# Performance work log

Hardware: AMD Instinct MI355X
Metric: run time of the kernel (lower is better)

## Reference

```python
import jax, jax.numpy as jnp
import numpy as np
from jax import lax

MODEL_DIM = 256
CTX_LEN = 48
CHUNK = 16
NUM_LAYERS = 4
NHEAD = 8
FF_DIM = 1024
EPS = 1e-5


def setup_inputs() -> dict:
    key = jax.random.key(0)
    ks = jax.random.split(key, 16)
    B, C, T = 16, MODEL_DIM, 1024
    s = 0.02
    inp = {
        "x": jax.random.normal(ks[0], (B, C, T), dtype=jnp.float32),
        "embedding": jax.random.normal(ks[1], (B, 2, C, 32), dtype=jnp.float32),
        "ctx_buf": jnp.zeros((B, NUM_LAYERS, CTX_LEN, C), dtype=jnp.float32),
        # per-layer stacked transformer-decoder-layer params
        "Wqkv": jax.random.normal(ks[2], (NUM_LAYERS, 3 * C, C), dtype=jnp.float32) * s,
        "bqkv": jnp.zeros((NUM_LAYERS, 3 * C), dtype=jnp.float32),
        "Wo": jax.random.normal(ks[3], (NUM_LAYERS, C, C), dtype=jnp.float32) * s,
        "bo": jnp.zeros((NUM_LAYERS, C), dtype=jnp.float32),
        "W1": jax.random.normal(ks[4], (NUM_LAYERS, FF_DIM, C), dtype=jnp.float32) * s,
        "b1": jnp.zeros((NUM_LAYERS, FF_DIM), dtype=jnp.float32),
        "W2": jax.random.normal(ks[5], (NUM_LAYERS, C, FF_DIM), dtype=jnp.float32) * s,
        "b2": jnp.zeros((NUM_LAYERS, C), dtype=jnp.float32),
        "ln1_g": jnp.ones((NUM_LAYERS, C), dtype=jnp.float32),
        "ln1_b": jnp.zeros((NUM_LAYERS, C), dtype=jnp.float32),
        "ln3_g": jnp.ones((NUM_LAYERS, C), dtype=jnp.float32),
        "ln3_b": jnp.zeros((NUM_LAYERS, C), dtype=jnp.float32),
    }
    return inp


def _layernorm(x, g, b):
    mu = jnp.mean(x, axis=-1, keepdims=True)
    var = jnp.mean(jnp.square(x - mu), axis=-1, keepdims=True)
    return (x - mu) * lax.rsqrt(var + EPS) * g + b


def _mha(q_in, kv_in, Wqkv, bqkv, Wo, bo):
    # q_in: [N, Lq, C], kv_in: [N, Lk, C]; torch nn.MultiheadAttention math (eval mode)
    C = q_in.shape[-1]
    dh = C // NHEAD
    Wq, Wk, Wv = jnp.split(Wqkv, 3, axis=0)
    bq, bk, bv = jnp.split(bqkv, 3)
    q = q_in @ Wq.T + bq
    k = kv_in @ Wk.T + bk
    v = kv_in @ Wv.T + bv
    N, Lq, _ = q.shape
    Lk = k.shape[1]
    q = q.reshape(N, Lq, NHEAD, dh)
    k = k.reshape(N, Lk, NHEAD, dh)
    v = v.reshape(N, Lk, NHEAD, dh)
    scores = jnp.einsum("nqhd,nkhd->nhqk", q, k) / jnp.sqrt(jnp.asarray(dh, q.dtype))
    attn = jax.nn.softmax(scores, axis=-1)
    out = jnp.einsum("nhqk,nkhd->nqhd", attn, v).reshape(N, Lq, C)
    return out @ Wo.T + bo


def _decoder_layer(tgt, Wqkv, bqkv, Wo, bo, W1, b1, W2, b2, ln1_g, ln1_b, ln3_g, ln3_b):
    # tgt: [N, ctx+chunk, C]; query = last `chunk` tokens; dropout=identity (eval)
    q = tgt[:, -CHUNK:, :]
    x1 = _layernorm(q + _mha(q, tgt, Wqkv, bqkv, Wo, bo), ln1_g, ln1_b)
    ff = jax.nn.relu(x1 @ W1.T + b1) @ W2.T + b2
    return _layernorm(x1 + ff, ln3_g, ln3_b)


def reference(x, embedding, ctx_buf, Wqkv, bqkv, Wo, bo, W1, b1, W2, b2,
              ln1_g, ln1_b, ln3_g, ln3_b):
    B, C, T = x.shape  # T multiple of CHUNK -> mod_pad is a no-op
    # ---- conv conditioning: per-(batch,channel) causal depthwise filter ----
    Le = embedding.shape[-1]
    filt = jnp.mean(embedding, axis=1).reshape(B * C, 1, Le)  # [B*C, 1, Le]
    inp = x.reshape(1, B * C, T)
    out = lax.conv_general_dilated(
        inp, filt, window_strides=(1,), padding=[(Le - 1, 0)],
        feature_group_count=B * C, dimension_numbers=("NCH", "OIH", "NCH"))
    output = out.reshape(B, C, T).transpose(0, 2, 1)  # [B, T, C]

    # ---- causal sliding-window decoder layers ----
    nwin = T // CHUNK
    W = CTX_LEN + CHUNK
    idx = jnp.arange(nwin)[:, None] * CHUNK + jnp.arange(W)[None, :]  # [nwin, W]
    for i in range(NUM_LAYERS):
        tgt_full = jnp.concatenate([ctx_buf[:, i], output], axis=1)  # [B, ctx+T, C]
        ctx_buf = ctx_buf.at[:, i].set(tgt_full[:, -CTX_LEN:])
        win = tgt_full[:, idx].reshape(B * nwin, W, C)  # unfold -> [B*nwin, W, C]
        chunks = _decoder_layer(win, Wqkv[i], bqkv[i], Wo[i], bo[i], W1[i], b1[i],
                                W2[i], b2[i], ln1_g[i], ln1_b[i], ln3_g[i], ln3_b[i])
        output = chunks.reshape(B, T, C)
    return output.transpose(0, 2, 1), ctx_buf
```

## Files before the change

### kernel.cpp

```cpp
#include <hip/hip_runtime.h>
#include <math.h>

#define BQ      16
#define CDIM    256
#define TLEN    1024
#define CTXL    48
#define CHUNKL  16
#define NLAYER  4
#define NHEADS  8
#define DHEAD   32
#define FFDIM   1024
#define NWIN    64
#define EXTL    1072
#define QKV_N   768

typedef __attribute__((ext_vector_type(4))) float floatx4;
typedef __attribute__((ext_vector_type(8))) __bf16 bf16x8;

__device__ __forceinline__ unsigned short f2bf(float f) {
    unsigned int u = __float_as_uint(f);
    u += 0x7fff + ((u >> 16) & 1);
    return (unsigned short)(u >> 16);
}
__device__ __forceinline__ float bf2f(unsigned short h) {
    return __uint_as_float(((unsigned int)h) << 16);
}

__global__ void f2b_multi_kernel(const float* __restrict__ p0,
                                 const float* __restrict__ p1,
                                 const float* __restrict__ p2,
                                 const float* __restrict__ p3,
                                 const float* __restrict__ p4,
                                 unsigned short* __restrict__ q0,
                                 unsigned short* __restrict__ q1,
                                 unsigned short* __restrict__ q2,
                                 unsigned short* __restrict__ q3,
                                 unsigned short* __restrict__ q4) {
    const int sizes[5] = {786432, 262144, 1048576, 1048576, 786432};
    const float* ins[5] = {p0, p1, p2, p3, p4};
    unsigned short* outs[5] = {q0, q1, q2, q3, q4};
    int seg = blockIdx.y;
    int i = (blockIdx.x * 256 + threadIdx.x) * 4;
    if (i < sizes[seg]) {
        float4 v = *(const float4*)(ins[seg] + i);
        ushort4 o;
        o.x = f2bf(v.x); o.y = f2bf(v.y); o.z = f2bf(v.z); o.w = f2bf(v.w);
        *(ushort4*)(outs[seg] + i) = o;
    }
}

__global__ void conv_kernel(const float* __restrict__ x,
                            const float* __restrict__ emb,
                            float* __restrict__ tmp) {
    int bc = blockIdx.x;
    int b = bc >> 8, c = bc & 255;
    __shared__ float xs[31 + TLEN];
    __shared__ float f[32];
    int t = threadIdx.x;
    if (t < 31) xs[t] = 0.f;
    const float* xrow = x + (size_t)bc * TLEN;
    for (int s = t; s < TLEN; s += 256) xs[31 + s] = xrow[s];
    if (t < 32) {
        const float* e0 = emb + (((size_t)b * 2 + 0) * CDIM + c) * 32;
        const float* e1 = emb + (((size_t)b * 2 + 1) * CDIM + c) * 32;
        f[t] = 0.5f * (e0[t] + e1[t]);
    }
    __syncthreads();
    float* orow = tmp + (size_t)bc * TLEN;
    for (int s = t; s < TLEN; s += 256) {
        float acc = 0.f;
#pragma unroll
        for (int l = 0; l < 32; ++l) acc += f[l] * xs[s + l];
        orow[s] = acc;
    }
}

__global__ void transpose_f2b_kernel(const float* __restrict__ in,
                                     unsigned short* __restrict__ out,
                                     float* __restrict__ ctxo,
                                     int R, int S) {
    __shared__ float tile[32][33];
    int b = blockIdx.z;
    int s0 = blockIdx.x * 32, r0 = blockIdx.y * 32;
    const float* inb = in + (size_t)b * R * S;
    unsigned short* outb = out + (size_t)b * R * S;
    int tx = threadIdx.x, ty = threadIdx.y;
    for (int i = ty; i < 32; i += 8)
        tile[i][tx] = inb[(size_t)(r0 + i) * S + s0 + tx];
    __syncthreads();
    for (int i = ty; i < 32; i += 8) {
        float v = tile[tx][i];
        int t = s0 + i, c = r0 + tx;
        outb[(size_t)t * R + c] = f2bf(v);
        if (t >= TLEN - CTXL)
            ctxo[(((size_t)b * NLAYER + 0) * CTXL + (t - (TLEN - CTXL)))
                 * CDIM + c] = v;
    }
}

__global__ void transpose_b2f_kernel(const unsigned short* __restrict__ in,
                                     float* __restrict__ out,
                                     int R, int S) {
    __shared__ float tile[32][33];
    int b = blockIdx.z;
    int s0 = blockIdx.x * 32, r0 = blockIdx.y * 32;
    const unsigned short* inb = in + (size_t)b * R * S;
    float* outb = out + (size_t)b * R * S;
    int tx = threadIdx.x, ty = threadIdx.y;
    for (int i = ty; i < 32; i += 8)
        tile[i][tx] = bf2f(inb[(size_t)(r0 + i) * S + s0 + tx]);
    __syncthreads();
    for (int i = ty; i < 32; i += 8)
        outb[(size_t)(s0 + i) * R + r0 + tx] = tile[tx][i];
}

template<int BM, int BN, int WM, int WN>
__global__ __launch_bounds__(256) void gemm_bf16_kernel(
    const unsigned short* __restrict__ A,
    const unsigned short* __restrict__ ctxb,
    int mode, int layer,
    const unsigned short* __restrict__ W,
    const float* __restrict__ bias,
    unsigned short* __restrict__ outb,
    int M, int N, int K, int relu) {
    constexpr int IA = BM / 32;
    constexpr int IB = BN / 32;
    constexpr int MT = WM / 16;
    constexpr int NTT = WN / 16;
    constexpr int NWX = BN / WN;
    __shared__ __align__(16) char smem[(BM + BN) * 128];
    char* smemA = smem;
    char* smemB = smem + BM * 128;
    int tid = threadIdx.x;
    int lane = tid & 63;
    int wid = tid >> 6;
    int ln = lane & 15, kq = lane >> 4;
    int wm = (wid / NWX) * WM, wn = (wid % NWX) * WN;
    int m0 = blockIdx.y * BM, n0 = blockIdx.x * BN;

    const unsigned short* arow[IA];
    int akc[IA];
    const unsigned short* brow[IB];
    int bkc[IB];
#pragma unroll
    for (int is = 0; is < IA; ++is) {
        int q = tid + is * 256;
        int m = q >> 3;
        akc[is] = ((q & 7) ^ (m & 7)) * 8;
        int mg = m0 + m;
        if (mode == 0) {
            arow[is] = A + (size_t)mg * K;
        } else {
            int b = mg / EXTL;
            int e = mg - b * EXTL;
            arow[is] = (e < CTXL)
                ? ctxb + (((size_t)b * NLAYER + layer) * CTXL + e) * CDIM
                : A + ((size_t)b * TLEN + (e - CTXL)) * CDIM;
        }
    }
#pragma unroll
    for (int is = 0; is < IB; ++is) {
        int q = tid + is * 256;
        int m = q >> 3;
        bkc[is] = ((q & 7) ^ (m & 7)) * 8;
        brow[is] = W + (size_t)(n0 + m) * K;
    }

    floatx4 acc[MT][NTT];
#pragma unroll
    for (int i = 0; i < MT; ++i)
#pragma unroll
        for (int j = 0; j < NTT; ++j) acc[i][j] = (floatx4){0.f, 0.f, 0.f, 0.f};

    for (int kt = 0; kt < K; kt += 64) {
#pragma unroll
        for (int is = 0; is < IA; ++is) {
            int off = (is * 256 + tid) * 16;
            __builtin_amdgcn_global_load_lds(
                (const __attribute__((address_space(1))) unsigned int*)
                    (const void*)(arow[is] + kt + akc[is]),
                (__attribute__((address_space(3))) unsigned int*)
                    (void*)(smemA + off), 16, 0, 0);
        }
#pragma unroll
        for (int is = 0; is < IB; ++is) {
            int off = (is * 256 + tid) * 16;
            __builtin_amdgcn_global_load_lds(
                (const __attribute__((address_space(1))) unsigned int*)
                    (const void*)(brow[is] + kt + bkc[is]),
                (__attribute__((address_space(3))) unsigned int*)
                    (void*)(smemB + off), 16, 0, 0);
        }
        __syncthreads();
#pragma unroll
        for (int s = 0; s < 2; ++s) {
            bf16x8 af[MT], bfv[NTT];
            int kc = s * 4 + kq;
#pragma unroll
            for (int i = 0; i < MT; ++i) {
                int ml = wm + 16 * i + ln;
                af[i] = *(const bf16x8*)(smemA + (ml * 8 + (kc ^ (ml & 7))) * 16);
            }
#pragma unroll
            for (int j = 0; j < NTT; ++j) {
                int nl = wn + 16 * j + ln;
                bfv[j] = *(const bf16x8*)(smemB + (nl * 8 + (kc ^ (nl & 7))) * 16);
            }
#pragma unroll
            for (int i = 0; i < MT; ++i)
#pragma unroll
                for (int j = 0; j < NTT; ++j)
                    acc[i][j] = __builtin_amdgcn_mfma_f32_16x16x32_bf16(
                        af[i], bfv[j], acc[i][j], 0, 0, 0);
        }
        __syncthreads();
    }

#pragma unroll
    for (int i = 0; i < MT; ++i) {
#pragma unroll
        for (int r = 0; r < 4; ++r) {
            int m = m0 + wm + 16 * i + kq * 4 + r;
#pragma unroll
            for (int j = 0; j < NTT; ++j) {
                int n = n0 + wn + 16 * j + ln;
                float v = acc[i][j][r] + bias[n];
                if (relu) v = fmaxf(v, 0.f);
                outb[(size_t)m * N + n] = f2bf(v);
            }
        }
    }
}

__global__ __launch_bounds__(256) void gemm_ln_kernel(
    const unsigned short* __restrict__ A,
    const unsigned short* __restrict__ W,
    const float* __restrict__ bias,
    const unsigned short* __restrict__ resid,
    const float* __restrict__ g,
    const float* __restrict__ beta,
    unsigned short* __restrict__ outb,
    float* __restrict__ ctxo, int clayer,
    int M, int K) {
    __shared__ __align__(16) unsigned short smA[32 * 64];
    __shared__ __align__(16) unsigned short smB[256 * 64];
    __shared__ float rsum[32][4];
    __shared__ float rsqs[32][4];
    int tid = threadIdx.x;
    int lane = tid & 63;
    int wid = tid >> 6;
    int ln = lane & 15, quad = lane >> 4;
    int wn = wid * 64;
    int m0 = blockIdx.x * 32;

    const unsigned short* arow =
        A + (size_t)(m0 + (tid >> 3)) * K + ((tid & 7) ^ ((tid >> 3) & 7)) * 8;
    const unsigned short* brow[8];
#pragma unroll
    for (int is = 0; is < 8; ++is) {
        int q = tid + is * 256;
        int mm = q >> 3;
        brow[is] = W + (size_t)mm * K + ((q & 7) ^ (mm & 7)) * 8;
    }

    floatx4 acc[2][4];
#pragma unroll
    for (int i = 0; i < 2; ++i)
#pragma unroll
        for (int j = 0; j < 4; ++j) acc[i][j] = (floatx4){0.f, 0.f, 0.f, 0.f};

    for (int kt = 0; kt < K; kt += 64) {
        __builtin_amdgcn_global_load_lds(
            (const __attribute__((address_space(1))) unsigned int*)
                (const void*)(arow + kt),
            (__attribute__((address_space(3))) unsigned int*)
                (void*)((char*)smA + tid * 16), 16, 0, 0);
#pragma unroll
        for (int is = 0; is < 8; ++is) {
            __builtin_amdgcn_global_load_lds(
                (const __attribute__((address_space(1))) unsigned int*)
                    (const void*)(brow[is] + kt),
                (__attribute__((address_space(3))) unsigned int*)
                    (void*)((char*)smB + (is * 256 + tid) * 16), 16, 0, 0);
        }
        __syncthreads();
#pragma unroll
        for (int s = 0; s < 2; ++s) {
            int kc = s * 4 + quad;
            bf16x8 af[2], bfv[4];
#pragma unroll
            for (int i = 0; i < 2; ++i) {
                int ml = 16 * i + ln;
                af[i] = *(const bf16x8*)(smA + (ml * 8 + (kc ^ (ml & 7))) * 8);
            }
#pragma unroll
            for (int j = 0; j < 4; ++j) {
                int nl = wn + 16 * j + ln;
                bfv[j] = *(const bf16x8*)(smB + (nl * 8 + (kc ^ (nl & 7))) * 8);
            }
#pragma unroll
            for (int i = 0; i < 2; ++i)
#pragma unroll
                for (int j = 0; j < 4; ++j)
                    acc[i][j] = __builtin_amdgcn_mfma_f32_16x16x32_bf16(
                        af[i], bfv[j], acc[i][j], 0, 0, 0);
        }
        __syncthreads();
    }

#pragma unroll
    for (int i = 0; i < 2; ++i)
#pragma unroll
        for (int r = 0; r < 4; ++r) {
            int m = m0 + 16 * i + quad * 4 + r;
#pragma unroll
            for (int j = 0; j < 4; ++j) {
                int n = wn + 16 * j + ln;
                acc[i][j][r] += bias[n] + bf2f(resid[(size_t)m * CDIM + n]);
            }
        }

#pragma unroll
    for (int i = 0; i < 2; ++i)
#pragma unroll
        for (int r = 0; r < 4; ++r) {
            float s1 = acc[i][0][r] + acc[i][1][r] + acc[i][2][r] + acc[i][3][r];
            float s2 = acc[i][0][r] * acc[i][0][r] + acc[i][1][r] * acc[i][1][r]
                     + acc[i][2][r] * acc[i][2][r] + acc[i][3][r] * acc[i][3][r];
#pragma unroll
            for (int off = 8; off >= 1; off >>= 1) {
                s1 += __shfl_xor(s1, off, 64);
                s2 += __shfl_xor(s2, off, 64);
            }
            if (ln == 0) {
                int row = 16 * i + quad * 4 + r;
                rsum[row][wid] = s1;
                rsqs[row][wid] = s2;
            }
        }
    __syncthreads();

#pragma unroll
    for (int i = 0; i < 2; ++i)
#pragma unroll
        for (int r = 0; r < 4; ++r) {
            int row = 16 * i + quad * 4 + r;
            float tot = rsum[row][0] + rsum[row][1] + rsum[row][2] + rsum[row][3];
            float tsq = rsqs[row][0] + rsqs[row][1] + rsqs[row][2] + rsqs[row][3];
            float mu = tot * (1.f / 256.f);
            float var = tsq * (1.f / 256.f) - mu * mu;
            float inv = rsqrtf(var + 1e-5f);
            int m = m0 + row;
            int t = m & (TLEN - 1), bb = m >> 10;
            bool wctx = (clayer >= 0) && (t >= TLEN - CTXL);
#pragma unroll
            for (int j = 0; j < 4; ++j) {
                int n = wn + 16 * j + ln;
                float y = (acc[i][j][r] - mu) * inv * g[n] + beta[n];
                outb[(size_t)m * CDIM + n] = f2bf(y);
                if (wctx)
                    ctxo[(((size_t)bb * NLAYER + clayer) * CTXL
                          + (t - (TLEN - CTXL))) * CDIM + n] = y;
            }
        }
}

__global__ __launch_bounds__(256) void attn_wo_ln_kernel(
    const unsigned short* __restrict__ QKV,
    const unsigned short* __restrict__ act,
    const unsigned short* __restrict__ Wo,
    const float* __restrict__ bo,
    const float* __restrict__ g,
    const float* __restrict__ beta,
    unsigned short* __restrict__ x1out) {
    int n = blockIdx.x, b = blockIdx.y;
    __shared__ __align__(16) unsigned short Vt[256][72];
    __shared__ __align__(16) unsigned short Pb[4][16][72];
    __shared__ __align__(16) unsigned short Ol[16][280];
    __shared__ float rsum[16][4];
    __shared__ float rsqs[16][4];
    int tid = threadIdx.x;
    int lane = tid & 63, wid = tid >> 6;
    int ln = lane & 15, quad = lane >> 4;
    int key0 = n * CHUNKL;
    const unsigned short* base = QKV + (size_t)b * EXTL * QKV_N;

    {
        int row = tid >> 2;
        int c0 = (tid & 3) * 64;
        const unsigned short* vrow =
            base + (size_t)(key0 + row) * QKV_N + 512 + c0;
#pragma unroll
        for (int s = 0; s < 8; ++s) {
            bf16x8 v = *(const bf16x8*)(vrow + 8 * s);
#pragma unroll
            for (int j = 0; j < 8; ++j)
                Vt[c0 + 8 * s + j][row] = ((const unsigned short*)&v)[j];
        }
    }
    __syncthreads();

    const float scale = 0.17677669529663687f;
#pragma unroll
    for (int hh = 0; hh < 2; ++hh) {
        int h = wid * 2 + hh;
        bf16x8 qf = *(const bf16x8*)(base
            + (size_t)(CTXL + key0 + ln) * QKV_N + h * DHEAD + quad * 8);
        floatx4 sc[4];
#pragma unroll
        for (int j = 0; j < 4; ++j) {
            bf16x8 kf = *(const bf16x8*)(base
                + (size_t)(key0 + j * 16 + ln) * QKV_N + 256
                + h * DHEAD + quad * 8);
            sc[j] = __builtin_amdgcn_mfma_f32_16x16x32_bf16(
                qf, kf, (floatx4){0.f, 0.f, 0.f, 0.f}, 0, 0, 0);
        }
        float p[4][4];
#pragma unroll
        for (int r = 0; r < 4; ++r) {
            float mx = -1e30f;
#pragma unroll
            for (int j = 0; j < 4; ++j) mx = fmaxf(mx, sc[j][r]);
            mx = fmaxf(mx, __shfl_xor(mx, 1, 64));
            mx = fmaxf(mx, __shfl_xor(mx, 2, 64));
            mx = fmaxf(mx, __shfl_xor(mx, 4, 64));
            mx = fmaxf(mx, __shfl_xor(mx, 8, 64));
            float sum = 0.f;
#pragma unroll
            for (int j = 0; j < 4; ++j) {
                float e = __expf((sc[j][r] - mx) * scale);
                p[r][j] = e;
                sum += e;
            }
            sum += __shfl_xor(sum, 1, 64);
            sum += __shfl_xor(sum, 2, 64);
            sum += __shfl_xor(sum, 4, 64);
            sum += __shfl_xor(sum, 8, 64);
            float inv = 1.f / sum;
#pragma unroll
            for (int j = 0; j < 4; ++j) p[r][j] *= inv;
        }
#pragma unroll
        for (int r = 0; r < 4; ++r)
#pragma unroll
            for (int j = 0; j < 4; ++j)
                Pb[wid][quad * 4 + r][j * 16 + ln] = f2bf(p[r][j]);
        bf16x8 pa0 = *(const bf16x8*)&Pb[wid][ln][quad * 8];
        bf16x8 pa1 = *(const bf16x8*)&Pb[wid][ln][32 + quad * 8];
#pragma unroll
        for (int jt = 0; jt < 2; ++jt) {
            bf16x8 v0 = *(const bf16x8*)&Vt[h * DHEAD + jt * 16 + ln][quad * 8];
            bf16x8 v1 = *(const bf16x8*)&Vt[h * DHEAD + jt * 16 + ln][32 + quad * 8];
            floatx4 a = __builtin_amdgcn_mfma_f32_16x16x32_bf16(
                pa0, v0, (floatx4){0.f, 0.f, 0.f, 0.f}, 0, 0, 0);
            a = __builtin_amdgcn_mfma_f32_16x16x32_bf16(pa1, v1, a, 0, 0, 0);
            int colb = wid * 64 + hh * 32 + jt * 16 + ln;
#pragma unroll
            for (int r = 0; r < 4; ++r)
                Ol[quad * 4 + r][colb] = f2bf(a[r]);
        }
    }
    __syncthreads();

    floatx4 o2[4];
#pragma unroll
    for (int j = 0; j < 4; ++j) o2[j] = (floatx4){0.f, 0.f, 0.f, 0.f};
#pragma unroll
    for (int s = 0; s < 8; ++s) {
        bf16x8 af = *(const bf16x8*)&Ol[ln][s * 32 + quad * 8];
#pragma unroll
        for (int j = 0; j < 4; ++j) {
            bf16x8 bv = *(const bf16x8*)(Wo
                + (size_t)(wid * 64 + j * 16 + ln) * CDIM + s * 32 + quad * 8);
            o2[j] = __builtin_amdgcn_mfma_f32_16x16x32_bf16(af, bv, o2[j], 0, 0, 0);
        }
    }

    const unsigned short* residb =
        act + ((size_t)b * TLEN + key0) * CDIM;
#pragma unroll
    for (int r = 0; r < 4; ++r) {
        int row = quad * 4 + r;
#pragma unroll
        for (int j = 0; j < 4; ++j) {
            int col = wid * 64 + j * 16 + ln;
            o2[j][r] += bo[col] + bf2f(residb[(size_t)row * CDIM + col]);
        }
    }

#pragma unroll
    for (int r = 0; r < 4; ++r) {
        float s1 = o2[0][r] + o2[1][r] + o2[2][r] + o2[3][r];
        float s2 = o2[0][r] * o2[0][r] + o2[1][r] * o2[1][r]
                 + o2[2][r] * o2[2][r] + o2[3][r] * o2[3][r];
#pragma unroll
        for (int off = 8; off >= 1; off >>= 1) {
            s1 += __shfl_xor(s1, off, 64);
            s2 += __shfl_xor(s2, off, 64);
        }
        if (ln == 0) {
            rsum[quad * 4 + r][wid] = s1;
            rsqs[quad * 4 + r][wid] = s2;
        }
    }
    __syncthreads();

    unsigned short* xout = x1out + ((size_t)b * TLEN + key0) * CDIM;
#pragma unroll
    for (int r = 0; r < 4; ++r) {
        int row = quad * 4 + r;
        float tot = rsum[row][0] + rsum[row][1] + rsum[row][2] + rsum[row][3];
        float tsq = rsqs[row][0] + rsqs[row][1] + rsqs[row][2] + rsqs[row][3];
        float mu = tot * (1.f / 256.f);
        float var = tsq * (1.f / 256.f) - mu * mu;
        float inv = rsqrtf(var + 1e-5f);
#pragma unroll
        for (int j = 0; j < 4; ++j) {
            int col = wid * 64 + j * 16 + ln;
            float y = (o2[j][r] - mu) * inv * g[col] + beta[col];
            xout[(size_t)row * CDIM + col] = f2bf(y);
        }
    }
}

extern "C" void kernel_launch(void* const* d_in, const int* in_sizes, int n_in,
                              void* d_out, int out_size, void* d_ws, size_t ws_size,
                              hipStream_t stream) {
    const float* x    = (const float*)d_in[0];
    const float* emb  = (const float*)d_in[1];
    const float* ctx  = (const float*)d_in[2];
    const float* Wqkv = (const float*)d_in[3];
    const float* bqkv = (const float*)d_in[4];
    const float* Wo   = (const float*)d_in[5];
    const float* bo   = (const float*)d_in[6];
    const float* W1   = (const float*)d_in[7];
    const float* b1   = (const float*)d_in[8];
    const float* W2   = (const float*)d_in[9];
    const float* b2   = (const float*)d_in[10];
    const float* ln1g = (const float*)d_in[11];
    const float* ln1b = (const float*)d_in[12];
    const float* ln3g = (const float*)d_in[13];
    const float* ln3b = (const float*)d_in[14];

    float* out = (float*)d_out;
    float* ctx_out = out + (size_t)BQ * CDIM * TLEN;

    char* w = (char*)d_ws;
    float* convt = (float*)w;         w += 16777216;
    unsigned short* actbf  = (unsigned short*)w; w += 8388608;
    unsigned short* x1bf   = (unsigned short*)w; w += 8388608;
    unsigned short* QKVbf  = (unsigned short*)w; w += 26345472;
    unsigned short* Hbf    = (unsigned short*)w; w += 33554432;
    unsigned short* ctxbf  = (unsigned short*)w; w += 1572864;
    unsigned short* Wqkvbf = (unsigned short*)w; w += 1572864;
    unsigned short* Wobf   = (unsigned short*)w; w += 524288;
    unsigned short* W1bf   = (unsigned short*)w; w += 2097152;
    unsigned short* W2bf   = (unsigned short*)w; w += 2097152;

    const int NT = BQ * TLEN;

    f2b_multi_kernel<<<dim3(1024, 5), 256, 0, stream>>>(
        Wqkv, Wo, W1, W2, ctx, Wqkvbf, Wobf, W1bf, W2bf, ctxbf);

    conv_kernel<<<BQ * CDIM, 256, 0, stream>>>(x, emb, convt);
    transpose_f2b_kernel<<<dim3(TLEN / 32, CDIM / 32, BQ), dim3(32, 8), 0,
                           stream>>>(convt, actbf, ctx_out, CDIM, TLEN);

    for (int i = 0; i < NLAYER; ++i) {
        const unsigned short* Wqkvb = Wqkvbf + (size_t)i * 3 * CDIM * CDIM;
        const float* bqi = bqkv + (size_t)i * 3 * CDIM;
        const unsigned short* Wob = Wobf + (size_t)i * CDIM * CDIM;
        const float* boi = bo + (size_t)i * CDIM;
        const unsigned short* W1b = W1bf + (size_t)i * FFDIM * CDIM;
        const float* b1i = b1 + (size_t)i * FFDIM;
        const unsigned short* W2b = W2bf + (size_t)i * CDIM * FFDIM;
        const float* b2i = b2 + (size_t)i * CDIM;

        gemm_bf16_kernel<128, 128, 64, 64><<<dim3(6, 134), 256, 0, stream>>>(
            actbf, ctxbf, 1, i, Wqkvb, bqi, QKVbf, BQ * EXTL, QKV_N, CDIM, 0);
        attn_wo_ln_kernel<<<dim3(NWIN, BQ), 256, 0, stream>>>(
            QKVbf, actbf, Wob, boi, ln1g + i * CDIM, ln1b + i * CDIM, x1bf);
        gemm_bf16_kernel<128, 128, 64, 64><<<dim3(8, 128), 256, 0, stream>>>(
            x1bf, nullptr, 0, i, W1b, b1i, Hbf, NT, FFDIM, CDIM, 1);
        gemm_ln_kernel<<<NT / 32, 256, 0, stream>>>(
            Hbf, W2b, b2i, x1bf, ln3g + i * CDIM, ln3b + i * CDIM,
            actbf, ctx_out, (i < NLAYER - 1) ? (i + 1) : -1, NT, FFDIM);
    }

    transpose_b2f_kernel<<<dim3(CDIM / 32, TLEN / 32, BQ), dim3(32, 8), 0,
                           stream>>>(actbf, out, TLEN, CDIM);
}
```

Before: 510.5 us.

## Fuse conv with transpose and enlarge gemm_ln row tile to 64

Replaces the separate depthwise conv and transpose kernels with one kernel that computes the causal filter per channel tile and writes bf16 [B,T,C] output directly, plus the ctx buffer tail. This removes the fp32 intermediate buffer round trip and one launch. It also doubles the M tile of the W2 GEMM+LayerNorm kernel from 32 to 64 rows, so each loaded W2 tile is reused across more rows, at the cost of more accumulator registers and half as many blocks. The attention kernel's Ol shared buffer padding is also reduced.

```diff
diff --git a/kernel.cpp b/kernel.cpp
--- a/kernel.cpp
+++ b/kernel.cpp
@@ -49,52 +49,56 @@
     }
 }
 
-__global__ void conv_kernel(const float* __restrict__ x,
-                            const float* __restrict__ emb,
-                            float* __restrict__ tmp) {
-    int bc = blockIdx.x;
-    int b = bc >> 8, c = bc & 255;
-    __shared__ float xs[31 + TLEN];
-    __shared__ float f[32];
-    int t = threadIdx.x;
-    if (t < 31) xs[t] = 0.f;
-    const float* xrow = x + (size_t)bc * TLEN;
-    for (int s = t; s < TLEN; s += 256) xs[31 + s] = xrow[s];
-    if (t < 32) {
-        const float* e0 = emb + (((size_t)b * 2 + 0) * CDIM + c) * 32;
-        const float* e1 = emb + (((size_t)b * 2 + 1) * CDIM + c) * 32;
-        f[t] = 0.5f * (e0[t] + e1[t]);
+__global__ __launch_bounds__(256) void conv_t_kernel(
+    const float* __restrict__ x, const float* __restrict__ emb,
+    unsigned short* __restrict__ actbf, float* __restrict__ ctxo) {
+    int t0 = blockIdx.x * 128;
+    int c0 = blockIdx.y * 32;
+    int b  = blockIdx.z;
+    __shared__ float xs[32][164];
+    __shared__ float filt[32][33];
+    int tid = threadIdx.x;
+
+#pragma unroll
+    for (int s = 0; s < 20; ++s) {
+        int li = tid + s * 256;
+        int c = li / 160, u = li - c * 160;
+        int gt = t0 + u - 31;
+        xs[c][u] = (gt >= 0 && gt < TLEN)
+            ? x[((size_t)b * CDIM + c0 + c) * TLEN + gt] : 0.f;
+    }
+#pragma unroll
+    for (int s = 0; s < 4; ++s) {
+        int li = tid + s * 256;
+        int c = li >> 5, l = li & 31;
+        const float* e0 = emb + (((size_t)b * 2 + 0) * CDIM + c0 + c) * 32;
+        const float* e1 = emb + (((size_t)b * 2 + 1) * CDIM + c0 + c) * 32;
+        filt[c][l] = 0.5f * (e0[l] + e1[l]);
     }
     __syncthreads();
-    float* orow = tmp + (size_t)bc * TLEN;
-    for (int s = t; s < TLEN; s += 256) {
+
+    int c = tid & 31;
+    int tb = tid >> 5;
+    float f[32];
+#pragma unroll
+    for (int l = 0; l < 32; ++l) f[l] = filt[c][l];
+    float4 xq[12];
+#pragma unroll
+    for (int s = 0; s < 12; ++s)
+        xq[s] = *(const float4*)&xs[c][tb * 16 + 4 * s];
+    const float* xv = (const float*)xq;
+
+    unsigned short* arow = actbf + ((size_t)b * TLEN + t0 + tb * 16) * CDIM + c0 + c;
+#pragma unroll
+    for (int t = 0; t < 16; ++t) {
         float acc = 0.f;
 #pragma unroll
-        for (int l = 0; l < 32; ++l) acc += f[l] * xs[s + l];
-        orow[s] = acc;
-    }
-}
-
-__global__ void transpose_f2b_kernel(const float* __restrict__ in,
-                                     unsigned short* __restrict__ out,
-                                     float* __restrict__ ctxo,
-                                     int R, int S) {
-    __shared__ float tile[32][33];
-    int b = blockIdx.z;
-    int s0 = blockIdx.x * 32, r0 = blockIdx.y * 32;
-    const float* inb = in + (size_t)b * R * S;
-    unsigned short* outb = out + (size_t)b * R * S;
-    int tx = threadIdx.x, ty = threadIdx.y;
-    for (int i = ty; i < 32; i += 8)
-        tile[i][tx] = inb[(size_t)(r0 + i) * S + s0 + tx];
-    __syncthreads();
-    for (int i = ty; i < 32; i += 8) {
-        float v = tile[tx][i];
-        int t = s0 + i, c = r0 + tx;
-        outb[(size_t)t * R + c] = f2bf(v);
-        if (t >= TLEN - CTXL)
-            ctxo[(((size_t)b * NLAYER + 0) * CTXL + (t - (TLEN - CTXL)))
-                 * CDIM + c] = v;
+        for (int l = 0; l < 32; ++l) acc += f[l] * xv[t + l];
+        arow[(size_t)t * CDIM] = f2bf(acc);
+        int gt = t0 + tb * 16 + t;
+        if (gt >= TLEN - CTXL)
+            ctxo[(((size_t)b * NLAYER + 0) * CTXL + (gt - (TLEN - CTXL)))
+                 * CDIM + c0 + c] = acc;
     }
 }
 
@@ -242,19 +246,26 @@
     unsigned short* __restrict__ outb,
     float* __restrict__ ctxo, int clayer,
     int M, int K) {
-    __shared__ __align__(16) unsigned short smA[32 * 64];
+    __shared__ __align__(16) unsigned short smA[64 * 64];
     __shared__ __align__(16) unsigned short smB[256 * 64];
-    __shared__ float rsum[32][4];
-    __shared__ float rsqs[32][4];
+    __shared__ float rsum[64][4];
+    __shared__ float rsqs[64][4];
     int tid = threadIdx.x;
     int lane = tid & 63;
     int wid = tid >> 6;
     int ln = lane & 15, quad = lane >> 4;
     int wn = wid * 64;
-    int m0 = blockIdx.x * 32;
-
-    const unsigned short* arow =
-        A + (size_t)(m0 + (tid >> 3)) * K + ((tid & 7) ^ ((tid >> 3) & 7)) * 8;
+    int m0 = blockIdx.x * 64;
+
+    const unsigned short* arow[2];
+    int akc[2];
+#pragma unroll
+    for (int is = 0; is < 2; ++is) {
+        int q = tid + is * 256;
+        int row = q >> 3;
+        akc[is] = ((q & 7) ^ (row & 7)) * 8;
+        arow[is] = A + (size_t)(m0 + row) * K;
+    }
     const unsigned short* brow[8];
 #pragma unroll
     for (int is = 0; is < 8; ++is) {
@@ -263,18 +274,21 @@
         brow[is] = W + (size_t)mm * K + ((q & 7) ^ (mm & 7)) * 8;
     }
 
-    floatx4 acc[2][4];
-#pragma unroll
-    for (int i = 0; i < 2; ++i)
+    floatx4 acc[4][4];
+#pragma unroll
+    for (int i = 0; i < 4; ++i)
 #pragma unroll
         for (int j = 0; j < 4; ++j) acc[i][j] = (floatx4){0.f, 0.f, 0.f, 0.f};
 
     for (int kt = 0; kt < K; kt += 64) {
-        __builtin_amdgcn_global_load_lds(
-            (const __attribute__((address_space(1))) unsigned int*)
-                (const void*)(arow + kt),
-            (__attribute__((address_space(3))) unsigned int*)
-                (void*)((char*)smA + tid * 16), 16, 0, 0);
+#pragma unroll
+        for (int is = 0; is < 2; ++is) {
+            __builtin_amdgcn_global_load_lds(
+                (const __attribute__((address_space(1))) unsigned int*)
+                    (const void*)(arow[is] + kt + akc[is]),
+                (__attribute__((address_space(3))) unsigned int*)
+                    (void*)((char*)smA + (is * 256 + tid) * 16), 16, 0, 0);
+        }
 #pragma unroll
         for (int is = 0; is < 8; ++is) {
             __builtin_amdgcn_global_load_lds(
@@ -287,9 +301,9 @@
 #pragma unroll
         for (int s = 0; s < 2; ++s) {
             int kc = s * 4 + quad;
-            bf16x8 af[2], bfv[4];
-#pragma unroll
-            for (int i = 0; i < 2; ++i) {
+            bf16x8 af[4], bfv[4];
+#pragma unroll
+            for (int i = 0; i < 4; ++i) {
                 int ml = 16 * i + ln;
                 af[i] = *(const bf16x8*)(smA + (ml * 8 + (kc ^ (ml & 7))) * 8);
             }
@@ -299,7 +313,7 @@
                 bfv[j] = *(const bf16x8*)(smB + (nl * 8 + (kc ^ (nl & 7))) * 8);
             }
 #pragma unroll
-            for (int i = 0; i < 2; ++i)
+            for (int i = 0; i < 4; ++i)
 #pragma unroll
                 for (int j = 0; j < 4; ++j)
                     acc[i][j] = __builtin_amdgcn_mfma_f32_16x16x32_bf16(
@@ -309,7 +323,7 @@
     }
 
 #pragma unroll
-    for (int i = 0; i < 2; ++i)
+    for (int i = 0; i < 4; ++i)
 #pragma unroll
         for (int r = 0; r < 4; ++r) {
             int m = m0 + 16 * i + quad * 4 + r;
@@ -321,7 +335,7 @@
         }
 
 #pragma unroll
-    for (int i = 0; i < 2; ++i)
+    for (int i = 0; i < 4; ++i)
 #pragma unroll
         for (int r = 0; r < 4; ++r) {
             float s1 = acc[i][0][r] + acc[i][1][r] + acc[i][2][r] + acc[i][3][r];
@@ -341,7 +355,7 @@
     __syncthreads();
 
 #pragma unroll
-    for (int i = 0; i < 2; ++i)
+    for (int i = 0; i < 4; ++i)
 #pragma unroll
         for (int r = 0; r < 4; ++r) {
             int row = 16 * i + quad * 4 + r;
@@ -376,7 +390,7 @@
     int n = blockIdx.x, b = blockIdx.y;
     __shared__ __align__(16) unsigned short Vt[256][72];
     __shared__ __align__(16) unsigned short Pb[4][16][72];
-    __shared__ __align__(16) unsigned short Ol[16][280];
+    __shared__ __align__(16) unsigned short Ol[16][264];
     __shared__ float rsum[16][4];
     __shared__ float rsqs[16][4];
     int tid = threadIdx.x;
@@ -546,7 +560,6 @@
     float* ctx_out = out + (size_t)BQ * CDIM * TLEN;
 
     char* w = (char*)d_ws;
-    float* convt = (float*)w;         w += 16777216;
     unsigned short* actbf  = (unsigned short*)w; w += 8388608;
     unsigned short* x1bf   = (unsigned short*)w; w += 8388608;
     unsigned short* QKVbf  = (unsigned short*)w; w += 26345472;
@@ -562,9 +575,8 @@
     f2b_multi_kernel<<<dim3(1024, 5), 256, 0, stream>>>(
         Wqkv, Wo, W1, W2, ctx, Wqkvbf, Wobf, W1bf, W2bf, ctxbf);
 
-    conv_kernel<<<BQ * CDIM, 256, 0, stream>>>(x, emb, convt);
-    transpose_f2b_kernel<<<dim3(TLEN / 32, CDIM / 32, BQ), dim3(32, 8), 0,
-                           stream>>>(convt, actbf, ctx_out, CDIM, TLEN);
+    conv_t_kernel<<<dim3(TLEN / 128, CDIM / 32, BQ), 256, 0, stream>>>(
+        x, emb, actbf, ctx_out);
 
     for (int i = 0; i < NLAYER; ++i) {
         const unsigned short* Wqkvb = Wqkvbf + (size_t)i * 3 * CDIM * CDIM;
@@ -582,7 +594,7 @@
             QKVbf, actbf, Wob, boi, ln1g + i * CDIM, ln1b + i * CDIM, x1bf);
         gemm_bf16_kernel<128, 128, 64, 64><<<dim3(8, 128), 256, 0, stream>>>(
             x1bf, nullptr, 0, i, W1b, b1i, Hbf, NT, FFDIM, CDIM, 1);
-        gemm_ln_kernel<<<NT / 32, 256, 0, stream>>>(
+        gemm_ln_kernel<<<NT / 64, 256, 0, stream>>>(
             Hbf, W2b, b2i, x1bf, ln3g + i * CDIM, ln3b + i * CDIM,
             actbf, ctx_out, (i < NLAYER - 1) ? (i + 1) : -1, NT, FFDIM);
     }
```

New measurement: 543.7 us. +6.5%, slower.
